# Kernel optimization log

Measured on AMD Instinct MI355X. Metric: run time of the kernel, lower is better.

Reference implementation:

```python
import jax, jax.numpy as jnp
import numpy as np

B, L, H, TE = 256, 2048, 64, 64  # batch, seq len, hidden_size, num_time_enc_dims


def _lin_init(k, out_d, in_d):
    bound = 1.0 / np.sqrt(in_d)
    kw, kb = jax.random.split(k)
    w = jax.random.uniform(kw, (out_d, in_d), jnp.float32, -bound, bound)
    b = jax.random.uniform(kb, (out_d,), jnp.float32, -bound, bound)
    return w, b


def setup_inputs() -> dict:
    key = jax.random.key(0)
    ks = jax.random.split(key, 16)
    x_xy = jax.random.normal(ks[0], (B, L, 2), jnp.float32)
    mask = jax.random.bernoulli(ks[1], 0.8, (B, L, 1)).astype(jnp.float32)  # 0 => masked position
    x = jnp.concatenate([x_xy, mask], axis=-1)  # (B,L,3)
    t = jax.random.uniform(ks[2], (B, L, 1), jnp.float32)
    te_w1, te_b1 = _lin_init(ks[3], TE, 1)
    te_w2, te_b2 = _lin_init(ks[4], TE, TE)
    fproj_w, fproj_b = _lin_init(ks[5], H, 3 + TE)
    bproj_w, bproj_b = _lin_init(ks[6], H, 3 + TE)
    fwz, fbz = _lin_init(ks[7], H, H)
    fwh, fbh = _lin_init(ks[8], H, H)
    bwz, bbz = _lin_init(ks[9], H, H)
    bwh, bbh = _lin_init(ks[10], H, H)
    head_hidden = max((2 * H + TE) // 2, 128)  # = 128
    gh_w1, gh_b1 = _lin_init(ks[11], head_hidden, 2 * H + TE)
    gh_w2, gh_b2 = _lin_init(ks[12], 1, head_hidden)
    mask_token = jnp.array([0.0, 0.01], jnp.float32) + jnp.array([0.1, 0.001], jnp.float32) * jax.random.normal(ks[13], (2,), jnp.float32)
    return dict(x=x, t=t, mask_token=mask_token,
                te_w1=te_w1, te_b1=te_b1, te_w2=te_w2, te_b2=te_b2,
                fproj_w=fproj_w, fproj_b=fproj_b, bproj_w=bproj_w, bproj_b=bproj_b,
                fwz=fwz, fbz=fbz, fwh=fwh, fbh=fbh,
                bwz=bwz, bbz=bbz, bwh=bwh, bbh=bbh,
                gh_w1=gh_w1, gh_b1=gh_b1, gh_w2=gh_w2, gh_b2=gh_b2)


def _mingru_prestates(inp, wz, bz, wh, bh, reverse):
    # inp: (B,L,H). Returns the hidden state BEFORE each step's update, in
    # time order, matching the torch code which stores h_* before cell.step.
    z = jax.nn.sigmoid(jnp.einsum('blh,oh->blo', inp, wz) + bz)
    h_tilde = jnp.tanh(jnp.einsum('blh,oh->blo', inp, wh) + bh)

    def step(h, zh):
        z_t, ht_t = zh
        return (1.0 - z_t) * h + z_t * ht_t, h  # emit pre-update carry

    h0 = jnp.zeros((inp.shape[0], wz.shape[0]), inp.dtype)
    _, hs = jax.lax.scan(step, h0,
                         (jnp.swapaxes(z, 0, 1), jnp.swapaxes(h_tilde, 0, 1)),
                         reverse=reverse)
    return jnp.swapaxes(hs, 0, 1)  # (B,L,H)


def reference(x, t, mask_token,
              te_w1, te_b1, te_w2, te_b2,
              fproj_w, fproj_b, bproj_w, bproj_b,
              fwz, fbz, fwh, fbh,
              bwz, bbz, bwh, bbh,
              gh_w1, gh_b1, gh_w2, gh_b2):
    mask_chan = x[..., 2:3]                      # (B,L,1)
    masked_pos = mask_chan == 0
    x_first2 = jnp.where(masked_pos, mask_token.reshape(1, 1, 2), x[..., :2])
    x3 = jnp.concatenate([x_first2, mask_chan], axis=-1)  # (B,L,3)

    t_enc = jax.nn.relu(jnp.einsum('blk,ok->blo', t, te_w1) + te_b1)
    t_enc = jnp.einsum('blk,ok->blo', t_enc, te_w2) + te_b2  # (B,L,TE)

    x_cat = jnp.concatenate([x3, t_enc], axis=-1)  # (B,L,3+TE)

    inp_fwd = jnp.einsum('blk,ok->blo', x_cat, fproj_w) + fproj_b
    inp_bwd = jnp.einsum('blk,ok->blo', x_cat, bproj_w) + bproj_b

    h_fwd = _mingru_prestates(inp_fwd, fwz, fbz, fwh, fbh, reverse=False)  # state after steps 0..t-1
    h_bwd = _mingru_prestates(inp_bwd, bwz, bbz, bwh, bbh, reverse=True)   # state after steps L-1..t+1

    h_fwd_final = h_fwd[:, -1:, :]  # state after steps 0..L-2
    h_bwd_final = h_bwd[:, 0:1, :]  # state after steps L-1..1

    unmasked = mask_chan > 0
    h_fwd_apply = jnp.where(unmasked, h_fwd, h_fwd_final)
    h_bwd_apply = jnp.where(unmasked, h_bwd, h_bwd_final)

    h_bi = jnp.concatenate([h_fwd_apply, h_bwd_apply, t_enc], axis=-1)  # (B,L,2H+TE)
    hid = jax.nn.relu(jnp.einsum('blk,ok->blo', h_bi, gh_w1) + gh_b1)
    preds = jnp.einsum('blk,ok->blo', hid, gh_w2) + gh_b2  # (B,L,1)
    return preds
```

## Files before the change

kernel.cpp:

```cpp
#include <hip/hip_runtime.h>
#include <stdint.h>

#define NB 256
#define NL 2048

typedef __attribute__((ext_vector_type(8))) short short8;
typedef __attribute__((ext_vector_type(4))) float f32x4;
#define MFMA16(a,b,c) __builtin_amdgcn_mfma_f32_16x16x32_bf16(a,b,c,0,0,0)

static __device__ __forceinline__ unsigned short f2bf(float f) {
    union { float f; uint32_t u; } v; v.f = f;
    uint32_t u = v.u;
    uint32_t r = u + 0x7fffu + ((u >> 16) & 1u);
    return (unsigned short)(r >> 16);
}
static __device__ __forceinline__ float bflo(uint32_t u) {
    union { uint32_t u; float f; } v; v.u = u << 16; return v.f;
}
static __device__ __forceinline__ float bfhi(uint32_t u) {
    union { uint32_t u; float f; } v; v.u = u & 0xffff0000u; return v.f;
}
#if __has_builtin(__builtin_amdgcn_cvt_pk_bf16_f32)
typedef __attribute__((ext_vector_type(2))) __bf16 bf16x2_t;
static __device__ __forceinline__ uint32_t pk2(float lo, float hi) {
    union { bf16x2_t v; uint32_t u; } c;
    c.v = __builtin_amdgcn_cvt_pk_bf16_f32(lo, hi);
    return c.u;
}
static __device__ __forceinline__ unsigned short bf1(float v) {
    union { bf16x2_t v; uint32_t u; } c;
    c.v = __builtin_amdgcn_cvt_pk_bf16_f32(v, v);
    return (unsigned short)(c.u & 0xffffu);
}
#else
static __device__ __forceinline__ uint32_t pk2(float lo, float hi) {
    return ((uint32_t)f2bf(hi) << 16) | (uint32_t)f2bf(lo);
}
static __device__ __forceinline__ unsigned short bf1(float v) { return f2bf(v); }
#endif
static __device__ __forceinline__ short8 frag8(const float* p) {
    short8 r;
#pragma unroll
    for (int j = 0; j < 8; ++j) r[j] = (short)f2bf(p[j]);
    return r;
}

#define TSTR 104

__global__ __launch_bounds__(256, 3) void prep_kernel(
    const float* __restrict__ x, const float* __restrict__ t,
    const float* __restrict__ mtok,
    const float* __restrict__ te_w1, const float* __restrict__ te_b1,
    const float* __restrict__ te_w2, const float* __restrict__ te_b2,
    const float* __restrict__ fpw, const float* __restrict__ fpb,
    const float* __restrict__ bpw, const float* __restrict__ bpb,
    const float* __restrict__ fwz, const float* __restrict__ fbz,
    const float* __restrict__ fwh, const float* __restrict__ fbh,
    const float* __restrict__ bwz, const float* __restrict__ bbz,
    const float* __restrict__ bwh, const float* __restrict__ bbh,
    int b0,
    uint32_t* __restrict__ abf,
    uint32_t* __restrict__ abb)
{
    __shared__ __align__(16) unsigned short s_te1[64*72];
    __shared__ __align__(16) unsigned short s_tenc[64*TSTR];
    __shared__ __align__(16) unsigned short s_inp[2][64*72];

    const int tid = threadIdx.x;
    const int w   = tid >> 6;
    const int l   = tid & 63;
    const int lq  = l >> 4;
    const int ln  = l & 15;

    short8 bte[2];
    {
        const float* row = te_w2 + (w*16 + ln)*64;
#pragma unroll
        for (int ks = 0; ks < 2; ++ks) bte[ks] = frag8(row + lq*8 + ks*32);
    }
    short8 bpj[2][3];
#pragma unroll
    for (int p = 0; p < 2; ++p) {
        const int g = 2*w + p;
        const float* PW = (g < 4) ? fpw : bpw;
        const float* row = PW + ((g & 3)*16 + ln)*67;
#pragma unroll
        for (int ks = 0; ks < 2; ++ks) {
            float tmp[8];
#pragma unroll
            for (int j = 0; j < 8; ++j) tmp[j] = row[3 + lq*8 + ks*32 + j];
            bpj[p][ks] = frag8(tmp);
        }
        {
            float tmp[8];
#pragma unroll
            for (int j = 0; j < 8; ++j) tmp[j] = (lq == 0 && j < 3) ? row[j] : 0.f;
            bpj[p][2] = frag8(tmp);
        }
    }
    const int wdir = w >> 1, wnp = w & 1;
    short8 bgz[2][2], bgh[2][2];
    float bias_gz[2], bias_gh[2];
    {
        const float* WZ = wdir ? bwz : fwz;
        const float* WH = wdir ? bwh : fwh;
        const float* BZ = wdir ? bbz : fbz;
        const float* BH = wdir ? bbh : fbh;
#pragma unroll
        for (int nt2 = 0; nt2 < 2; ++nt2) {
            const int nt = wnp*2 + nt2;
            const float* rz = WZ + (nt*16 + ln)*64;
            const float* rh = WH + (nt*16 + ln)*64;
#pragma unroll
            for (int ks = 0; ks < 2; ++ks) {
                bgz[nt2][ks] = frag8(rz + lq*8 + ks*32);
                bgh[nt2][ks] = frag8(rh + lq*8 + ks*32);
            }
            bias_gz[nt2] = BZ[nt*16 + ln];
            bias_gh[nt2] = BH[nt*16 + ln];
        }
    }
    const float bias_te = te_b2[w*16 + ln];
    float bias_pj[2];
#pragma unroll
    for (int p = 0; p < 2; ++p) {
        const int g = 2*w + p;
        bias_pj[p] = ((g < 4) ? fpb : bpb)[(g & 3)*16 + ln];
    }
    const float mt0 = mtok[0], mt1 = mtok[1];

    const int baseposl = blockIdx.x * 256;

    auto P0 = [&](int ch) {
        const int gbase = (b0 << 11) + baseposl + ch*64;
        const int pos = tid & 63;
        const float tv = t[gbase + pos];
        const int k0 = (tid >> 6) * 16;
        uint32_t* dst = (uint32_t*)(s_te1 + pos*72 + k0);
#pragma unroll
        for (int kk = 0; kk < 16; kk += 2) {
            float v0 = fmaxf(fmaf(tv, te_w1[k0+kk],   te_b1[k0+kk]),   0.f);
            float v1 = fmaxf(fmaf(tv, te_w1[k0+kk+1], te_b1[k0+kk+1]), 0.f);
            dst[kk >> 1] = pk2(v0, v1);
        }
        if (tid < 64) {
            const float* xp = x + (size_t)(gbase + tid)*3;
            const float mc = xp[2];
            const float x0 = (mc == 0.f) ? mt0 : xp[0];
            const float x1 = (mc == 0.f) ? mt1 : xp[1];
            uint32_t* xr = (uint32_t*)(s_tenc + tid*TSTR + 64);
            xr[0] = pk2(x0, x1);
            xr[1] = pk2(mc, 0.f);
        }
    };
    auto G1 = [&]() {
        const int o = w*16 + ln;
#pragma unroll
        for (int mt = 0; mt < 4; ++mt) {
            f32x4 c = {0.f, 0.f, 0.f, 0.f};
#pragma unroll
            for (int ks = 0; ks < 2; ++ks) {
                const short8 a = *(const short8*)(s_te1 + (mt*16+ln)*72 + lq*8 + ks*32);
                c = MFMA16(a, bte[ks], c);
            }
#pragma unroll
            for (int r = 0; r < 4; ++r) {
                const int m = mt*16 + lq*4 + r;
                s_tenc[m*TSTR + o] = bf1(c[r] + bias_te);
            }
        }
    };
    auto G2 = [&]() {
#pragma unroll
        for (int mt = 0; mt < 4; ++mt) {
            const unsigned short* arow = s_tenc + (mt*16+ln)*TSTR + lq*8;
            short8 a0 = *(const short8*)(arow);
            short8 a1 = *(const short8*)(arow + 32);
            short8 a2 = *(const short8*)(arow + 64);
#pragma unroll
            for (int p = 0; p < 2; ++p) {
                const int g = 2*w + p;
                const int dir = g >> 2;
                const int o = (g & 3)*16 + ln;
                f32x4 c = {0.f, 0.f, 0.f, 0.f};
                c = MFMA16(a0, bpj[p][0], c);
                c = MFMA16(a1, bpj[p][1], c);
                c = MFMA16(a2, bpj[p][2], c);
#pragma unroll
                for (int r = 0; r < 4; ++r) {
                    const int m = mt*16 + lq*4 + r;
                    s_inp[dir][m*72 + o] = bf1(c[r] + bias_pj[p]);
                }
            }
        }
    };
    auto G3 = [&](int ch) {
        const int chbase = baseposl + ch*64;
        const int ll0 = chbase & 2047;
        const int bl  = chbase >> 11;
        uint32_t* abD = (wdir ? abb : abf) + (size_t)(bl*64)*NL + ll0;
#pragma unroll
        for (int mt = 0; mt < 4; ++mt) {
            const short8 a0 = *(const short8*)(s_inp[wdir] + (mt*16+ln)*72 + lq*8);
            const short8 a1 = *(const short8*)(s_inp[wdir] + (mt*16+ln)*72 + lq*8 + 32);
#pragma unroll
            for (int nt2 = 0; nt2 < 2; ++nt2) {
                f32x4 cz = {0.f, 0.f, 0.f, 0.f};
                f32x4 ch2 = {0.f, 0.f, 0.f, 0.f};
                cz  = MFMA16(a0, bgz[nt2][0], cz);
                cz  = MFMA16(a1, bgz[nt2][1], cz);
                ch2 = MFMA16(a0, bgh[nt2][0], ch2);
                ch2 = MFMA16(a1, bgh[nt2][1], ch2);
                const int o = (wnp*2 + nt2)*16 + ln;
                uint4 v;
                uint32_t* vp = (uint32_t*)&v;
#pragma unroll
                for (int r = 0; r < 4; ++r) {
                    const float az = cz[r]  + bias_gz[nt2];
                    const float ah = ch2[r] + bias_gh[nt2];
                    const float z  = __builtin_amdgcn_rcpf(1.f + __expf(-az));
                    const float cc = fminf(fmaxf(ah, -15.f), 15.f);
                    const float e2 = __expf(2.f * cc);
                    const float th = 1.f - 2.f * __builtin_amdgcn_rcpf(e2 + 1.f);
                    vp[r] = pk2(1.f - z, z * th);
                }
                *(uint4*)(abD + (size_t)o*NL + mt*16 + lq*4) = v;
            }
        }
    };

#pragma unroll 1
    for (int i = tid; i < 64*14; i += 256) {
        const int row = i / 14, c = i % 14;
        ((uint32_t*)s_tenc)[row*(TSTR/2) + 34 + c] = 0;
    }
    P0(0);
    __syncthreads();
    G1();
    __syncthreads();
    G2();
    __syncthreads();
#pragma unroll 1
    for (int ch = 0; ch < 4; ++ch) {
        G3(ch);
        if (ch < 3) P0(ch + 1);
        __syncthreads();
        if (ch < 3) {
            G1();
            __syncthreads();
            G2();
            __syncthreads();
        }
    }
}

#define SSTR 129

__global__ __launch_bounds__(256) void scan3_kernel(
    const uint32_t* __restrict__ abf, const uint32_t* __restrict__ abb,
    unsigned short* __restrict__ hf, unsigned short* __restrict__ hb)
{
    __shared__ uint32_t s_seg[32*SSTR];
    __shared__ float s_A[8][33], s_B[8][33], s_Hin[8][33];
    __shared__ float s_H[32];

    const int rl  = blockIdx.x >> 2;
    const int dir = (blockIdx.x >> 1) & 1;
    const int h0  = (blockIdx.x & 1) * 32;
    const int tid = threadIdx.x;
    const int h   = tid & 31;
    const int q   = tid >> 5;

    const uint32_t* ab = (dir ? abb : abf) + (size_t)rl * 64 * NL + (size_t)h0 * NL;
    unsigned short* out = (dir ? hb : hf) + (size_t)rl * NL * 64 + h0;

    if (tid < 32) s_H[tid] = 0.f;
    __syncthreads();

#pragma unroll 1
    for (int si = 0; si < 16; ++si) {
        const int s  = dir ? (15 - si) : si;
        const int l0 = s * 128;

#pragma unroll
        for (int rep = 0; rep < 16; ++rep) {
            const int idx = rep*256 + tid;
            const int hh = idx >> 7, xx = idx & 127;
            s_seg[hh*SSTR + xx] = ab[(size_t)hh*NL + l0 + xx];
        }
        __syncthreads();

        uint32_t regs[16];
        float A = 1.f, Bc = 0.f;
#pragma unroll
        for (int i = 0; i < 16; ++i) {
            const int g = q*16 + i;
            const int xx = dir ? (127 - g) : g;
            const uint32_t uab = s_seg[h*SSTR + xx];
            regs[i] = uab;
            Bc = fmaf(bflo(uab), Bc, bfhi(uab));
            A *= bflo(uab);
        }
        s_A[q][h] = A; s_B[q][h] = Bc;
        __syncthreads();

        if (tid < 32) {
            float H = s_H[tid];
#pragma unroll
            for (int qq = 0; qq < 8; ++qq) {
                s_Hin[qq][tid] = H;
                H = fmaf(s_A[qq][tid], H, s_B[qq][tid]);
            }
            s_H[tid] = H;
        }
        __syncthreads();

        float hv = s_Hin[q][h];
#pragma unroll
        for (int i = 0; i < 16; ++i) {
            const int g = q*16 + i;
            const int xx = dir ? (127 - g) : g;
            const uint32_t uab = regs[i];
            out[(size_t)(l0 + xx)*64 + h] = bf1(hv);
            hv = fmaf(bflo(uab), hv, bfhi(uab));
        }
        __syncthreads();
    }
}

__global__ __launch_bounds__(256, 3) void head_kernel(
    const float* __restrict__ x, const float* __restrict__ t,
    const float* __restrict__ te_w1, const float* __restrict__ te_b1,
    const float* __restrict__ te_w2, const float* __restrict__ te_b2,
    const unsigned short* __restrict__ hf, const unsigned short* __restrict__ hb,
    const float* __restrict__ w1, const float* __restrict__ b1,
    const float* __restrict__ w2, const float* __restrict__ b2,
    int b0,
    float* __restrict__ out)
{
    __shared__ __align__(16) unsigned short s_a[64*200];
    __shared__ __align__(16) unsigned short s_te1[64*72];
    __shared__ float s_part[4][64];
    __shared__ float s_mc[64];

    const int tid = threadIdx.x;
    const int w   = tid >> 6;
    const int l   = tid & 63;
    const int lq  = l >> 4;
    const int ln  = l & 15;

    short8 bw1[2][6];
    float b1v[2], w2v[2];
#pragma unroll
    for (int p = 0; p < 2; ++p) {
        const int o = (2*w + p)*16 + ln;
        const float* row = w1 + o*192;
#pragma unroll
        for (int ks = 0; ks < 6; ++ks) bw1[p][ks] = frag8(row + lq*8 + ks*32);
        b1v[p] = b1[o];
        w2v[p] = w2[o];
    }
    short8 bte[2];
    {
        const float* row = te_w2 + (w*16 + ln)*64;
#pragma unroll
        for (int ks = 0; ks < 2; ++ks) bte[ks] = frag8(row + lq*8 + ks*32);
    }
    const float bias_te = te_b2[w*16 + ln];
    const float bias2 = b2[0];

    const int baseposl = blockIdx.x * 256;

    auto A = [&](int ch) {
        const int gbase = (b0 << 11) + baseposl + ch*64;
        if (tid < 64) s_mc[tid] = x[(size_t)(gbase + tid)*3 + 2];
        const int pos = tid & 63;
        const float tv = t[gbase + pos];
        const int k0 = (tid >> 6) * 16;
        uint32_t* dst = (uint32_t*)(s_te1 + pos*72 + k0);
#pragma unroll
        for (int kk = 0; kk < 16; kk += 2) {
            float v0 = fmaxf(fmaf(tv, te_w1[k0+kk],   te_b1[k0+kk]),   0.f);
            float v1 = fmaxf(fmaf(tv, te_w1[k0+kk+1], te_b1[k0+kk+1]), 0.f);
            dst[kk >> 1] = pk2(v0, v1);
        }
    };
    auto Bp = [&](int ch) {
        const int chbase = baseposl + ch*64;
        const int ll0 = chbase & 2047;
        const int bl  = chbase >> 11;
        const size_t rowbase = (size_t)bl * NL * 64;
#pragma unroll
        for (int rep = 0; rep < 4; ++rep) {
            const int idx = rep*256 + tid;
            const int seg = idx >> 9;
            const int row = (idx >> 3) & 63;
            const int c   = idx & 7;
            const bool unm = s_mc[row] > 0.f;
            const uint4* src = (seg == 0)
                ? (const uint4*)(hf + rowbase + (size_t)(unm ? (ll0+row) : (NL-1))*64)
                : (const uint4*)(hb + rowbase + (size_t)(unm ? (ll0+row) : 0)*64);
            ((uint4*)s_a)[row*25 + seg*8 + c] = src[c];
        }
        const int o = w*16 + ln;
#pragma unroll
        for (int mt = 0; mt < 4; ++mt) {
            f32x4 c = {0.f, 0.f, 0.f, 0.f};
#pragma unroll
            for (int ks = 0; ks < 2; ++ks) {
                const short8 a = *(const short8*)(s_te1 + (mt*16+ln)*72 + lq*8 + ks*32);
                c = MFMA16(a, bte[ks], c);
            }
#pragma unroll
            for (int r = 0; r < 4; ++r) {
                const int m = mt*16 + lq*4 + r;
                s_a[m*200 + 128 + o] = bf1(c[r] + bias_te);
            }
        }
    };
    auto Cp = [&]() {
#pragma unroll
        for (int mt = 0; mt < 4; ++mt) {
            short8 af[6];
#pragma unroll
            for (int ks = 0; ks < 6; ++ks)
                af[ks] = *(const short8*)(s_a + (mt*16+ln)*200 + lq*8 + ks*32);
            float vs[4] = {0.f, 0.f, 0.f, 0.f};
#pragma unroll
            for (int p = 0; p < 2; ++p) {
                f32x4 c = {0.f, 0.f, 0.f, 0.f};
#pragma unroll
                for (int ks = 0; ks < 6; ++ks) c = MFMA16(af[ks], bw1[p][ks], c);
#pragma unroll
                for (int r = 0; r < 4; ++r)
                    vs[r] += fmaxf(c[r] + b1v[p], 0.f) * w2v[p];
            }
#pragma unroll
            for (int mask = 1; mask < 16; mask <<= 1) {
#pragma unroll
                for (int r = 0; r < 4; ++r)
                    vs[r] += __shfl_xor(vs[r], mask);
            }
            if (ln == 0) {
#pragma unroll
                for (int r = 0; r < 4; ++r)
                    s_part[w][mt*16 + lq*4 + r] = vs[r];
            }
        }
    };
    auto Dp = [&](int ch) {
        const int gbase = (b0 << 11) + baseposl + ch*64;
        if (tid < 64) {
            out[gbase + tid] = s_part[0][tid] + s_part[1][tid]
                             + s_part[2][tid] + s_part[3][tid] + bias2;
        }
    };

    A(0);
    __syncthreads();
#pragma unroll 1
    for (int ch = 0; ch < 4; ++ch) {
        Bp(ch);
        __syncthreads();
        Cp();
        __syncthreads();
        Dp(ch);
        if (ch < 3) A(ch + 1);
        __syncthreads();
    }
}

extern "C" void kernel_launch(void* const* d_in, const int* in_sizes, int n_in,
                              void* d_out, int out_size, void* d_ws, size_t ws_size,
                              hipStream_t stream)
{
    const float* x     = (const float*)d_in[0];
    const float* t     = (const float*)d_in[1];
    const float* mtok  = (const float*)d_in[2];
    const float* te_w1 = (const float*)d_in[3];
    const float* te_b1 = (const float*)d_in[4];
    const float* te_w2 = (const float*)d_in[5];
    const float* te_b2 = (const float*)d_in[6];
    const float* fpw   = (const float*)d_in[7];
    const float* fpb   = (const float*)d_in[8];
    const float* bpw   = (const float*)d_in[9];
    const float* bpb   = (const float*)d_in[10];
    const float* fwz   = (const float*)d_in[11];
    const float* fbz   = (const float*)d_in[12];
    const float* fwh   = (const float*)d_in[13];
    const float* fbh   = (const float*)d_in[14];
    const float* bwz   = (const float*)d_in[15];
    const float* bbz   = (const float*)d_in[16];
    const float* bwh   = (const float*)d_in[17];
    const float* bbh   = (const float*)d_in[18];
    const float* w1    = (const float*)d_in[19];
    const float* b1    = (const float*)d_in[20];
    const float* w2    = (const float*)d_in[21];
    const float* b2    = (const float*)d_in[22];

    const size_t per_b = 1572864ull;
    int Bg = NB;
    while ((size_t)Bg * per_b > ws_size && Bg > 1) Bg >>= 1;
    const int nG = NB / Bg;

    char* ws = (char*)d_ws;
    uint32_t*       abf  = (uint32_t*)(ws);
    uint32_t*       abb  = abf + (size_t)Bg * 64 * NL;
    unsigned short* hf   = (unsigned short*)(abb + (size_t)Bg * 64 * NL);
    unsigned short* hb   = hf + (size_t)Bg * NL * 64;

    for (int g = 0; g < nG; ++g) {
        const int b0 = g * Bg;

        prep_kernel<<<8 * Bg, 256, 0, stream>>>(
            x, t, mtok, te_w1, te_b1, te_w2, te_b2,
            fpw, fpb, bpw, bpb, fwz, fbz, fwh, fbh, bwz, bbz, bwh, bbh,
            b0, abf, abb);

        scan3_kernel<<<4 * Bg, 256, 0, stream>>>(abf, abb, hf, hb);

        head_kernel<<<8 * Bg, 256, 0, stream>>>(
            x, t, te_w1, te_b1, te_w2, te_b2,
            hf, hb, w1, b1, w2, b2, b0, (float*)d_out);
    }
}
```

Before: 380.3 us.

## Fuse next group's prep with current group's head into one launch

Prep and head bodies become device functions that share one union of shared-memory layouts. A new fused kernel runs the prep blocks for group g+1 alongside the head blocks for group g in a single grid, so the two independent stages can overlap and one launch per group is saved. This only matters when the workspace forces more than one batch group. With a single group, the change mostly gives head_kernel a larger shared-memory footprint and a 3-blocks-per-SM launch bound, which could lower its occupancy.

Result: slower. 562.1 us (+47.8%).

```diff
diff --git a/kernel.cpp b/kernel.cpp
--- a/kernel.cpp
+++ b/kernel.cpp
@@ -47,7 +47,23 @@
 
 #define TSTR 104
 
-__global__ __launch_bounds__(256, 3) void prep_kernel(
+struct PrepShm {
+    unsigned short te1[64*72];
+    unsigned short tenc[64*TSTR];
+    unsigned short inp[2][64*72];
+};
+struct HeadShm {
+    unsigned short a[64*200];
+    unsigned short te1[64*72];
+    float part[4][64];
+    float mc[64];
+};
+union Shm {
+    PrepShm p;
+    HeadShm h;
+};
+
+static __device__ void prep_body(Shm& u,
     const float* __restrict__ x, const float* __restrict__ t,
     const float* __restrict__ mtok,
     const float* __restrict__ te_w1, const float* __restrict__ te_b1,
@@ -58,13 +74,11 @@
     const float* __restrict__ fwh, const float* __restrict__ fbh,
     const float* __restrict__ bwz, const float* __restrict__ bbz,
     const float* __restrict__ bwh, const float* __restrict__ bbh,
-    int b0,
-    uint32_t* __restrict__ abf,
-    uint32_t* __restrict__ abb)
-{
-    __shared__ __align__(16) unsigned short s_te1[64*72];
-    __shared__ __align__(16) unsigned short s_tenc[64*TSTR];
-    __shared__ __align__(16) unsigned short s_inp[2][64*72];
+    int b0, int blk,
+    uint32_t* __restrict__ abf, uint32_t* __restrict__ abb)
+{
+    unsigned short* s_te1  = u.p.te1;
+    unsigned short* s_tenc = u.p.tenc;
 
     const int tid = threadIdx.x;
     const int w   = tid >> 6;
@@ -129,7 +143,7 @@
     }
     const float mt0 = mtok[0], mt1 = mtok[1];
 
-    const int baseposl = blockIdx.x * 256;
+    const int baseposl = blk * 256;
 
     auto P0 = [&](int ch) {
         const int gbase = (b0 << 11) + baseposl + ch*64;
@@ -189,7 +203,7 @@
 #pragma unroll
                 for (int r = 0; r < 4; ++r) {
                     const int m = mt*16 + lq*4 + r;
-                    s_inp[dir][m*72 + o] = bf1(c[r] + bias_pj[p]);
+                    u.p.inp[dir][m*72 + o] = bf1(c[r] + bias_pj[p]);
                 }
             }
         }
@@ -201,8 +215,8 @@
         uint32_t* abD = (wdir ? abb : abf) + (size_t)(bl*64)*NL + ll0;
 #pragma unroll
         for (int mt = 0; mt < 4; ++mt) {
-            const short8 a0 = *(const short8*)(s_inp[wdir] + (mt*16+ln)*72 + lq*8);
-            const short8 a1 = *(const short8*)(s_inp[wdir] + (mt*16+ln)*72 + lq*8 + 32);
+            const short8 a0 = *(const short8*)(u.p.inp[wdir] + (mt*16+ln)*72 + lq*8);
+            const short8 a1 = *(const short8*)(u.p.inp[wdir] + (mt*16+ln)*72 + lq*8 + 32);
 #pragma unroll
             for (int nt2 = 0; nt2 < 2; ++nt2) {
                 f32x4 cz = {0.f, 0.f, 0.f, 0.f};
@@ -254,6 +268,194 @@
     }
 }
 
+static __device__ void head_body(Shm& u,
+    const float* __restrict__ x, const float* __restrict__ t,
+    const float* __restrict__ te_w1, const float* __restrict__ te_b1,
+    const float* __restrict__ te_w2, const float* __restrict__ te_b2,
+    const unsigned short* __restrict__ hf, const unsigned short* __restrict__ hb,
+    const float* __restrict__ w1, const float* __restrict__ b1,
+    const float* __restrict__ w2, const float* __restrict__ b2,
+    int b0, int blk,
+    float* __restrict__ out)
+{
+    unsigned short* s_a   = u.h.a;
+    unsigned short* s_te1 = u.h.te1;
+
+    const int tid = threadIdx.x;
+    const int w   = tid >> 6;
+    const int l   = tid & 63;
+    const int lq  = l >> 4;
+    const int ln  = l & 15;
+
+    short8 bw1[2][6];
+    float b1v[2], w2v[2];
+#pragma unroll
+    for (int p = 0; p < 2; ++p) {
+        const int o = (2*w + p)*16 + ln;
+        const float* row = w1 + o*192;
+#pragma unroll
+        for (int ks = 0; ks < 6; ++ks) bw1[p][ks] = frag8(row + lq*8 + ks*32);
+        b1v[p] = b1[o];
+        w2v[p] = w2[o];
+    }
+    short8 bte[2];
+    {
+        const float* row = te_w2 + (w*16 + ln)*64;
+#pragma unroll
+        for (int ks = 0; ks < 2; ++ks) bte[ks] = frag8(row + lq*8 + ks*32);
+    }
+    const float bias_te = te_b2[w*16 + ln];
+    const float bias2 = b2[0];
+
+    const int baseposl = blk * 256;
+
+    auto A = [&](int ch) {
+        const int gbase = (b0 << 11) + baseposl + ch*64;
+        if (tid < 64) u.h.mc[tid] = x[(size_t)(gbase + tid)*3 + 2];
+        const int pos = tid & 63;
+        const float tv = t[gbase + pos];
+        const int k0 = (tid >> 6) * 16;
+        uint32_t* dst = (uint32_t*)(s_te1 + pos*72 + k0);
+#pragma unroll
+        for (int kk = 0; kk < 16; kk += 2) {
+            float v0 = fmaxf(fmaf(tv, te_w1[k0+kk],   te_b1[k0+kk]),   0.f);
+            float v1 = fmaxf(fmaf(tv, te_w1[k0+kk+1], te_b1[k0+kk+1]), 0.f);
+            dst[kk >> 1] = pk2(v0, v1);
+        }
+    };
+    auto Bp = [&](int ch) {
+        const int chbase = baseposl + ch*64;
+        const int ll0 = chbase & 2047;
+        const int bl  = chbase >> 11;
+        const size_t rowbase = (size_t)bl * NL * 64;
+#pragma unroll
+        for (int rep = 0; rep < 4; ++rep) {
+            const int idx = rep*256 + tid;
+            const int seg = idx >> 9;
+            const int row = (idx >> 3) & 63;
+            const int c   = idx & 7;
+            const bool unm = u.h.mc[row] > 0.f;
+            const uint4* src = (seg == 0)
+                ? (const uint4*)(hf + rowbase + (size_t)(unm ? (ll0+row) : (NL-1))*64)
+                : (const uint4*)(hb + rowbase + (size_t)(unm ? (ll0+row) : 0)*64);
+            ((uint4*)s_a)[row*25 + seg*8 + c] = src[c];
+        }
+        const int o = w*16 + ln;
+#pragma unroll
+        for (int mt = 0; mt < 4; ++mt) {
+            f32x4 c = {0.f, 0.f, 0.f, 0.f};
+#pragma unroll
+            for (int ks = 0; ks < 2; ++ks) {
+                const short8 a = *(const short8*)(s_te1 + (mt*16+ln)*72 + lq*8 + ks*32);
+                c = MFMA16(a, bte[ks], c);
+            }
+#pragma unroll
+            for (int r = 0; r < 4; ++r) {
+                const int m = mt*16 + lq*4 + r;
+                s_a[m*200 + 128 + o] = bf1(c[r] + bias_te);
+            }
+        }
+    };
+    auto Cp = [&]() {
+#pragma unroll
+        for (int mt = 0; mt < 4; ++mt) {
+            short8 af[6];
+#pragma unroll
+            for (int ks = 0; ks < 6; ++ks)
+                af[ks] = *(const short8*)(s_a + (mt*16+ln)*200 + lq*8 + ks*32);
+            float vs[4] = {0.f, 0.f, 0.f, 0.f};
+#pragma unroll
+            for (int p = 0; p < 2; ++p) {
+                f32x4 c = {0.f, 0.f, 0.f, 0.f};
+#pragma unroll
+                for (int ks = 0; ks < 6; ++ks) c = MFMA16(af[ks], bw1[p][ks], c);
+#pragma unroll
+                for (int r = 0; r < 4; ++r)
+                    vs[r] += fmaxf(c[r] + b1v[p], 0.f) * w2v[p];
+            }
+#pragma unroll
+            for (int mask = 1; mask < 16; mask <<= 1) {
+#pragma unroll
+                for (int r = 0; r < 4; ++r)
+                    vs[r] += __shfl_xor(vs[r], mask);
+            }
+            if (ln == 0) {
+#pragma unroll
+                for (int r = 0; r < 4; ++r)
+                    u.h.part[w][mt*16 + lq*4 + r] = vs[r];
+            }
+        }
+    };
+    auto Dp = [&](int ch) {
+        const int gbase = (b0 << 11) + baseposl + ch*64;
+        if (tid < 64) {
+            out[gbase + tid] = u.h.part[0][tid] + u.h.part[1][tid]
+                             + u.h.part[2][tid] + u.h.part[3][tid] + bias2;
+        }
+    };
+
+    A(0);
+    __syncthreads();
+#pragma unroll 1
+    for (int ch = 0; ch < 4; ++ch) {
+        Bp(ch);
+        __syncthreads();
+        Cp();
+        __syncthreads();
+        Dp(ch);
+        if (ch < 3) A(ch + 1);
+        __syncthreads();
+    }
+}
+
+__global__ __launch_bounds__(256, 3) void prep_kernel(
+    const float* x, const float* t, const float* mtok,
+    const float* te_w1, const float* te_b1, const float* te_w2, const float* te_b2,
+    const float* fpw, const float* fpb, const float* bpw, const float* bpb,
+    const float* fwz, const float* fbz, const float* fwh, const float* fbh,
+    const float* bwz, const float* bbz, const float* bwh, const float* bbh,
+    int b0, uint32_t* abf, uint32_t* abb)
+{
+    __shared__ __align__(16) Shm u;
+    prep_body(u, x, t, mtok, te_w1, te_b1, te_w2, te_b2,
+              fpw, fpb, bpw, bpb, fwz, fbz, fwh, fbh, bwz, bbz, bwh, bbh,
+              b0, blockIdx.x, abf, abb);
+}
+
+__global__ __launch_bounds__(256, 3) void head_kernel(
+    const float* x, const float* t,
+    const float* te_w1, const float* te_b1, const float* te_w2, const float* te_b2,
+    const unsigned short* hf, const unsigned short* hb,
+    const float* w1, const float* b1, const float* w2, const float* b2,
+    int b0, float* out)
+{
+    __shared__ __align__(16) Shm u;
+    head_body(u, x, t, te_w1, te_b1, te_w2, te_b2, hf, hb,
+              w1, b1, w2, b2, b0, blockIdx.x, out);
+}
+
+__global__ __launch_bounds__(256, 3) void fused_kernel(
+    const float* x, const float* t, const float* mtok,
+    const float* te_w1, const float* te_b1, const float* te_w2, const float* te_b2,
+    const float* fpw, const float* fpb, const float* bpw, const float* bpb,
+    const float* fwz, const float* fbz, const float* fwh, const float* fbh,
+    const float* bwz, const float* bbz, const float* bwh, const float* bbh,
+    const unsigned short* hf, const unsigned short* hb,
+    const float* w1, const float* b1, const float* w2, const float* b2,
+    int b0_head, int b0_prep, int nPrep,
+    uint32_t* abf, uint32_t* abb, float* out)
+{
+    __shared__ __align__(16) Shm u;
+    if ((int)blockIdx.x < nPrep) {
+        prep_body(u, x, t, mtok, te_w1, te_b1, te_w2, te_b2,
+                  fpw, fpb, bpw, bpb, fwz, fbz, fwh, fbh, bwz, bbz, bwh, bbh,
+                  b0_prep, blockIdx.x, abf, abb);
+    } else {
+        head_body(u, x, t, te_w1, te_b1, te_w2, te_b2, hf, hb,
+                  w1, b1, w2, b2, b0_head, blockIdx.x - nPrep, out);
+    }
+}
+
 #define SSTR 129
 
 __global__ __launch_bounds__(256) void scan3_kernel(
@@ -324,148 +526,6 @@
             out[(size_t)(l0 + xx)*64 + h] = bf1(hv);
             hv = fmaf(bflo(uab), hv, bfhi(uab));
         }
-        __syncthreads();
-    }
-}
-
-__global__ __launch_bounds__(256, 3) void head_kernel(
-    const float* __restrict__ x, const float* __restrict__ t,
-    const float* __restrict__ te_w1, const float* __restrict__ te_b1,
-    const float* __restrict__ te_w2, const float* __restrict__ te_b2,
-    const unsigned short* __restrict__ hf, const unsigned short* __restrict__ hb,
-    const float* __restrict__ w1, const float* __restrict__ b1,
-    const float* __restrict__ w2, const float* __restrict__ b2,
-    int b0,
-    float* __restrict__ out)
-{
-    __shared__ __align__(16) unsigned short s_a[64*200];
-    __shared__ __align__(16) unsigned short s_te1[64*72];
-    __shared__ float s_part[4][64];
-    __shared__ float s_mc[64];
-
-    const int tid = threadIdx.x;
-    const int w   = tid >> 6;
-    const int l   = tid & 63;
-    const int lq  = l >> 4;
-    const int ln  = l & 15;
-
-    short8 bw1[2][6];
-    float b1v[2], w2v[2];
-#pragma unroll
-    for (int p = 0; p < 2; ++p) {
-        const int o = (2*w + p)*16 + ln;
-        const float* row = w1 + o*192;
-#pragma unroll
-        for (int ks = 0; ks < 6; ++ks) bw1[p][ks] = frag8(row + lq*8 + ks*32);
-        b1v[p] = b1[o];
-        w2v[p] = w2[o];
-    }
-    short8 bte[2];
-    {
-        const float* row = te_w2 + (w*16 + ln)*64;
-#pragma unroll
-        for (int ks = 0; ks < 2; ++ks) bte[ks] = frag8(row + lq*8 + ks*32);
-    }
-    const float bias_te = te_b2[w*16 + ln];
-    const float bias2 = b2[0];
-
-    const int baseposl = blockIdx.x * 256;
-
-    auto A = [&](int ch) {
-        const int gbase = (b0 << 11) + baseposl + ch*64;
-        if (tid < 64) s_mc[tid] = x[(size_t)(gbase + tid)*3 + 2];
-        const int pos = tid & 63;
-        const float tv = t[gbase + pos];
-        const int k0 = (tid >> 6) * 16;
-        uint32_t* dst = (uint32_t*)(s_te1 + pos*72 + k0);
-#pragma unroll
-        for (int kk = 0; kk < 16; kk += 2) {
-            float v0 = fmaxf(fmaf(tv, te_w1[k0+kk],   te_b1[k0+kk]),   0.f);
-            float v1 = fmaxf(fmaf(tv, te_w1[k0+kk+1], te_b1[k0+kk+1]), 0.f);
-            dst[kk >> 1] = pk2(v0, v1);
-        }
-    };
-    auto Bp = [&](int ch) {
-        const int chbase = baseposl + ch*64;
-        const int ll0 = chbase & 2047;
-        const int bl  = chbase >> 11;
-        const size_t rowbase = (size_t)bl * NL * 64;
-#pragma unroll
-        for (int rep = 0; rep < 4; ++rep) {
-            const int idx = rep*256 + tid;
-            const int seg = idx >> 9;
-            const int row = (idx >> 3) & 63;
-            const int c   = idx & 7;
-            const bool unm = s_mc[row] > 0.f;
-            const uint4* src = (seg == 0)
-                ? (const uint4*)(hf + rowbase + (size_t)(unm ? (ll0+row) : (NL-1))*64)
-                : (const uint4*)(hb + rowbase + (size_t)(unm ? (ll0+row) : 0)*64);
-            ((uint4*)s_a)[row*25 + seg*8 + c] = src[c];
-        }
-        const int o = w*16 + ln;
-#pragma unroll
-        for (int mt = 0; mt < 4; ++mt) {
-            f32x4 c = {0.f, 0.f, 0.f, 0.f};
-#pragma unroll
-            for (int ks = 0; ks < 2; ++ks) {
-                const short8 a = *(const short8*)(s_te1 + (mt*16+ln)*72 + lq*8 + ks*32);
-                c = MFMA16(a, bte[ks], c);
-            }
-#pragma unroll
-            for (int r = 0; r < 4; ++r) {
-                const int m = mt*16 + lq*4 + r;
-                s_a[m*200 + 128 + o] = bf1(c[r] + bias_te);
-            }
-        }
-    };
-    auto Cp = [&]() {
-#pragma unroll
-        for (int mt = 0; mt < 4; ++mt) {
-            short8 af[6];
-#pragma unroll
-            for (int ks = 0; ks < 6; ++ks)
-                af[ks] = *(const short8*)(s_a + (mt*16+ln)*200 + lq*8 + ks*32);
-            float vs[4] = {0.f, 0.f, 0.f, 0.f};
-#pragma unroll
-            for (int p = 0; p < 2; ++p) {
-                f32x4 c = {0.f, 0.f, 0.f, 0.f};
-#pragma unroll
-                for (int ks = 0; ks < 6; ++ks) c = MFMA16(af[ks], bw1[p][ks], c);
-#pragma unroll
-                for (int r = 0; r < 4; ++r)
-                    vs[r] += fmaxf(c[r] + b1v[p], 0.f) * w2v[p];
-            }
-#pragma unroll
-            for (int mask = 1; mask < 16; mask <<= 1) {
-#pragma unroll
-                for (int r = 0; r < 4; ++r)
-                    vs[r] += __shfl_xor(vs[r], mask);
-            }
-            if (ln == 0) {
-#pragma unroll
-                for (int r = 0; r < 4; ++r)
-                    s_part[w][mt*16 + lq*4 + r] = vs[r];
-            }
-        }
-    };
-    auto Dp = [&](int ch) {
-        const int gbase = (b0 << 11) + baseposl + ch*64;
-        if (tid < 64) {
-            out[gbase + tid] = s_part[0][tid] + s_part[1][tid]
-                             + s_part[2][tid] + s_part[3][tid] + bias2;
-        }
-    };
-
-    A(0);
-    __syncthreads();
-#pragma unroll 1
-    for (int ch = 0; ch < 4; ++ch) {
-        Bp(ch);
-        __syncthreads();
-        Cp();
-        __syncthreads();
-        Dp(ch);
-        if (ch < 3) A(ch + 1);
         __syncthreads();
     }
 }
@@ -509,18 +569,25 @@
     unsigned short* hf   = (unsigned short*)(abb + (size_t)Bg * 64 * NL);
     unsigned short* hb   = hf + (size_t)Bg * NL * 64;
 
+    prep_kernel<<<8 * Bg, 256, 0, stream>>>(
+        x, t, mtok, te_w1, te_b1, te_w2, te_b2,
+        fpw, fpb, bpw, bpb, fwz, fbz, fwh, fbh, bwz, bbz, bwh, bbh,
+        0, abf, abb);
+
     for (int g = 0; g < nG; ++g) {
-        const int b0 = g * Bg;
-
-        prep_kernel<<<8 * Bg, 256, 0, stream>>>(
-            x, t, mtok, te_w1, te_b1, te_w2, te_b2,
-            fpw, fpb, bpw, bpb, fwz, fbz, fwh, fbh, bwz, bbz, bwh, bbh,
-            b0, abf, abb);
-
         scan3_kernel<<<4 * Bg, 256, 0, stream>>>(abf, abb, hf, hb);
 
-        head_kernel<<<8 * Bg, 256, 0, stream>>>(
-            x, t, te_w1, te_b1, te_w2, te_b2,
-            hf, hb, w1, b1, w2, b2, b0, (float*)d_out);
-    }
-}
+        if (g < nG - 1) {
+            fused_kernel<<<16 * Bg, 256, 0, stream>>>(
+                x, t, mtok, te_w1, te_b1, te_w2, te_b2,
+                fpw, fpb, bpw, bpb, fwz, fbz, fwh, fbh, bwz, bbz, bwh, bbh,
+                hf, hb, w1, b1, w2, b2,
+                g * Bg, (g + 1) * Bg, 8 * Bg,
+                abf, abb, (float*)d_out);
+        } else {
+            head_kernel<<<8 * Bg, 256, 0, stream>>>(
+                x, t, te_w1, te_b1, te_w2, te_b2,
+                hf, hb, w1, b1, w2, b2, g * Bg, (float*)d_out);
+        }
+    }
+}
```
